# Kernel tuning notes

Hardware: AMD Instinct MI355X
Metric: run time of the kernel (lower is better)

## Reference

```python
import jax, jax.numpy as jnp
import numpy as np

EMB_DIM = 128
HEAD_SIZE = 16  # embDim // numHea = 128 // 8


def setup_inputs() -> dict:
    key = jax.random.key(0)
    k1, k2, k3, k4 = jax.random.split(key, 4)
    B, T = 8, 2048
    inpEmb = jax.random.normal(k1, (B, T, EMB_DIM), dtype=jnp.float32)
    # nn.Linear(embDim, heaSiz, bias=False) weights, stored transposed so y = x @ W
    Wq = jax.random.normal(k2, (EMB_DIM, HEAD_SIZE), dtype=jnp.float32) / np.sqrt(EMB_DIM)
    Wk = jax.random.normal(k3, (EMB_DIM, HEAD_SIZE), dtype=jnp.float32) / np.sqrt(EMB_DIM)
    Wv = jax.random.normal(k4, (EMB_DIM, HEAD_SIZE), dtype=jnp.float32) / np.sqrt(EMB_DIM)
    return {"inpEmb": inpEmb, "Wq": Wq, "Wk": Wk, "Wv": Wv}


def reference(inpEmb, Wq, Wk, Wv):
    # q,k,v: [B, T, H]
    q = inpEmb @ Wq
    k = inpEmb @ Wk
    v = inpEmb @ Wv
    scale = HEAD_SIZE ** -0.5
    # scores: [B, T, T]
    scores = jnp.einsum('bqh,bkh->bqk', q, k) * scale
    T = inpEmb.shape[1]
    causal = jnp.tril(jnp.ones((T, T), dtype=bool))
    scores = jnp.where(causal, scores, -jnp.inf)
    weights = jax.nn.softmax(scores, axis=-1)
    # dropout treated as identity (eval mode) for deterministic reference
    return jnp.einsum('bqk,bkh->bqh', weights, v)
```

## Files before the change

### kernel.cpp

```cpp
#include <hip/hip_runtime.h>
#include <hip/hip_bf16.h>

#define T_SEQ 2048
#define EMB   128
#define H     16
#define BATCH 8
#define BQ    64

typedef short short8_t __attribute__((ext_vector_type(8)));
typedef float f32x4    __attribute__((ext_vector_type(4)));

__device__ __forceinline__ unsigned short f2bf(float f) {
    __hip_bfloat16 h = __float2bfloat16(f);
    return *reinterpret_cast<unsigned short*>(&h);
}

__global__ __launch_bounds__(256) void qkv_kernel(
    const float* __restrict__ x,
    const float* __restrict__ Wq,
    const float* __restrict__ Wk,
    const float* __restrict__ Wv,
    unsigned short* __restrict__ Qbf,
    unsigned short* __restrict__ Kbf,
    unsigned short* __restrict__ Vt)
{
    __shared__ float Wt[3][16][132];

    const int tid = threadIdx.x;
    const int r0  = blockIdx.x * 32;

#pragma unroll
    for (int p = 0; p < 6; ++p) {
        const int idx4 = tid + p * 256;
        const int flat = idx4 * 4;
        const int mm   = flat >> 11;
        const int rem  = flat & 2047;
        const int d    = rem >> 4;
        const int c0   = rem & 15;
        const float* Wm = (mm == 0) ? Wq : (mm == 1) ? Wk : Wv;
        float4 w = *reinterpret_cast<const float4*>(Wm + rem);
        Wt[mm][c0    ][d] = w.x;
        Wt[mm][c0 + 1][d] = w.y;
        Wt[mm][c0 + 2][d] = w.z;
        Wt[mm][c0 + 3][d] = w.w;
    }
    __syncthreads();

    const int col  = tid & 15;
    const int rg   = tid >> 4;
    const int rowA = r0 + 2 * rg;
    const int rowB = rowA + 1;
    const float* xA = x + (size_t)rowA * EMB;
    const float* xB = x + (size_t)rowB * EMB;

    float qa0 = 0.f, ka0 = 0.f, va0 = 0.f;
    float qa1 = 0.f, ka1 = 0.f, va1 = 0.f;
#pragma unroll
    for (int d0 = 0; d0 < 128; d0 += 4) {
        float4 a  = *reinterpret_cast<const float4*>(xA + d0);
        float4 bb = *reinterpret_cast<const float4*>(xB + d0);
        float4 wq = *reinterpret_cast<const float4*>(&Wt[0][col][d0]);
        float4 wk = *reinterpret_cast<const float4*>(&Wt[1][col][d0]);
        float4 wv = *reinterpret_cast<const float4*>(&Wt[2][col][d0]);
        qa0 += a.x*wq.x + a.y*wq.y + a.z*wq.z + a.w*wq.w;
        ka0 += a.x*wk.x + a.y*wk.y + a.z*wk.z + a.w*wk.w;
        va0 += a.x*wv.x + a.y*wv.y + a.z*wv.z + a.w*wv.w;
        qa1 += bb.x*wq.x + bb.y*wq.y + bb.z*wq.z + bb.w*wq.w;
        ka1 += bb.x*wk.x + bb.y*wk.y + bb.z*wk.z + bb.w*wk.w;
        va1 += bb.x*wv.x + bb.y*wv.y + bb.z*wv.z + bb.w*wv.w;
    }
    const int bA = rowA >> 11, iA = rowA & 2047;
    const int bB = rowB >> 11, iB = rowB & 2047;
    Qbf[(size_t)rowA * H + col] = f2bf(qa0 * 0.25f);
    Kbf[(size_t)rowA * H + col] = f2bf(ka0);
    Vt[((size_t)bA * H + col) * T_SEQ + iA] = f2bf(va0);
    Qbf[(size_t)rowB * H + col] = f2bf(qa1 * 0.25f);
    Kbf[(size_t)rowB * H + col] = f2bf(ka1);
    Vt[((size_t)bB * H + col) * T_SEQ + iB] = f2bf(va1);
}

__global__ __launch_bounds__(256) void attn_phase1(
    const unsigned short* __restrict__ Qbf,
    const unsigned short* __restrict__ Kbf,
    const unsigned short* __restrict__ Vt,
    float* __restrict__ P2, int cs, int maxp)
{
    __shared__ unsigned int Pbuf[4][32][17];

    const int qt   = blockIdx.x;
    const int cch  = blockIdx.y;
    const int b    = blockIdx.z;
    const int i0   = qt * BQ;
    const int kbeg = cch << cs;
    if (kbeg >= i0 + BQ) return;

    const int tid  = threadIdx.x;
    const int w    = tid >> 6;
    const int lane = tid & 63;
    const int q    = lane >> 4;
    const int n    = lane & 15;
    const int irow = i0 + w * 16 + n;
    const int kend = min(kbeg + (1 << cs), i0 + w * 16 + 16);
    const int ntiles = (kend - kbeg + 63) >> 6;

    const unsigned short* Qp = Qbf + (size_t)b * T_SEQ * H;
    const unsigned short* Kp = Kbf + (size_t)b * T_SEQ * H;
    const unsigned short* Vp = Vt  + (size_t)b * H * T_SEQ;

    short8_t qf = {0,0,0,0,0,0,0,0};
    if (q < 2)
        qf = *reinterpret_cast<const short8_t*>(Qp + (size_t)irow * H + q * 8);

    f32x4 acc = {0.f, 0.f, 0.f, 0.f};
    float m = -1e30f, l = 0.f;

    for (int kt = 0; kt < ntiles; ++kt) {
        const int j0 = kbeg + kt * 64;

        f32x4 S[4];
#pragma unroll
        for (int s = 0; s < 4; ++s) {
            short8_t kf = {0,0,0,0,0,0,0,0};
            if (q < 2)
                kf = *reinterpret_cast<const short8_t*>(
                        Kp + (size_t)(j0 + s * 16 + n) * H + q * 8);
            f32x4 z = {0.f, 0.f, 0.f, 0.f};
            S[s] = __builtin_amdgcn_mfma_f32_16x16x32_bf16(kf, qf, z, 0, 0, 0);
        }

        float tm = -1e30f;
#pragma unroll
        for (int s = 0; s < 4; ++s) {
            const int kb = j0 + s * 16 + q * 4;
#pragma unroll
            for (int r = 0; r < 4; ++r) {
                float v = (kb + r <= irow) ? S[s][r] : -1e30f;
                S[s][r] = v;
                tm = fmaxf(tm, v);
            }
        }
        tm = fmaxf(tm, __shfl_xor(tm, 16));
        tm = fmaxf(tm, __shfl_xor(tm, 32));
        const float mn    = fmaxf(m, tm);
        const float alpha = __expf(m - mn);
        m = mn;

        float ps = 0.f;
#pragma unroll
        for (int s = 0; s < 4; ++s) {
            float e0 = __expf(S[s][0] - mn);
            float e1 = __expf(S[s][1] - mn);
            float e2 = __expf(S[s][2] - mn);
            float e3 = __expf(S[s][3] - mn);
            ps += (e0 + e1) + (e2 + e3);
            unsigned int b0 = __builtin_bit_cast(unsigned int, e0);
            unsigned int b1 = __builtin_bit_cast(unsigned int, e1);
            unsigned int b2 = __builtin_bit_cast(unsigned int, e2);
            unsigned int b3 = __builtin_bit_cast(unsigned int, e3);
            Pbuf[w][s * 8 + q * 2 + 0][n] = (b1 & 0xffff0000u) | (b0 >> 16);
            Pbuf[w][s * 8 + q * 2 + 1][n] = (b3 & 0xffff0000u) | (b2 >> 16);
        }
        ps += __shfl_xor(ps, 16);
        ps += __shfl_xor(ps, 32);
        l = l * alpha + ps;
        acc[0] *= alpha; acc[1] *= alpha; acc[2] *= alpha; acc[3] *= alpha;

#pragma unroll
        for (int h = 0; h < 2; ++h) {
            short8_t vf = *reinterpret_cast<const short8_t*>(
                    Vp + (size_t)n * T_SEQ + (j0 + h * 32 + q * 8));
            union { unsigned int u[4]; short8_t v; } pu;
            pu.u[0] = Pbuf[w][h * 16 + q * 4 + 0][n];
            pu.u[1] = Pbuf[w][h * 16 + q * 4 + 1][n];
            pu.u[2] = Pbuf[w][h * 16 + q * 4 + 2][n];
            pu.u[3] = Pbuf[w][h * 16 + q * 4 + 3][n];
            acc = __builtin_amdgcn_mfma_f32_16x16x32_bf16(vf, pu.v, acc, 0, 0, 0);
        }
    }

    float* pp = P2 + ((size_t)(b * T_SEQ + irow) * maxp + cch) * 18;
    float2 r01; r01.x = acc[0]; r01.y = acc[1];
    float2 r23; r23.x = acc[2]; r23.y = acc[3];
    *reinterpret_cast<float2*>(pp + q * 4)     = r01;
    *reinterpret_cast<float2*>(pp + q * 4 + 2) = r23;
    if (q == 0) { pp[16] = m; pp[17] = l; }
}

__global__ __launch_bounds__(256) void attn_phase2(
    const float* __restrict__ P2, float* __restrict__ out, int cs, int maxp)
{
    const int gid = blockIdx.x * 256 + threadIdx.x;
    const int row = gid >> 4;
    const int d   = gid & 15;
    const int ib  = row & (T_SEQ - 1);
    const int nc  = (ib >> cs) + 1;
    const float* base = P2 + (size_t)row * maxp * 18;

    float M = -1e30f;
    for (int p = 0; p < nc; ++p) M = fmaxf(M, base[p * 18 + 16]);
    float L = 0.f, o = 0.f;
    for (int p = 0; p < nc; ++p) {
        const float wgt = __expf(base[p * 18 + 16] - M);
        L += wgt * base[p * 18 + 17];
        o += wgt * base[p * 18 + d];
    }
    out[gid] = o / L;
}

extern "C" void kernel_launch(void* const* d_in, const int* in_sizes, int n_in,
                              void* d_out, int out_size, void* d_ws, size_t ws_size,
                              hipStream_t stream)
{
    const float* x  = (const float*)d_in[0];
    const float* Wq = (const float*)d_in[1];
    const float* Wk = (const float*)d_in[2];
    const float* Wv = (const float*)d_in[3];
    float* out = (float*)d_out;

    const size_t NE = (size_t)BATCH * T_SEQ * H;
    unsigned short* Qbf = (unsigned short*)d_ws;
    unsigned short* Kbf = Qbf + NE;
    unsigned short* Vt  = Kbf + NE;
    float* P2 = (float*)(Vt + NE);

    const size_t need8 = 3 * NE * 2 + (size_t)BATCH * T_SEQ * 8 * 18 * 4;
    int cs, maxp;
    if (ws_size >= need8) { cs = 8; maxp = 8; }
    else                  { cs = 9; maxp = 4; }

    qkv_kernel<<<BATCH * T_SEQ / 32, 256, 0, stream>>>(x, Wq, Wk, Wv, Qbf, Kbf, Vt);
    attn_phase1<<<dim3(T_SEQ / BQ, maxp, BATCH), 256, 0, stream>>>(
        Qbf, Kbf, Vt, P2, cs, maxp);
    attn_phase2<<<(int)(NE / 256), 256, 0, stream>>>(P2, out, cs, maxp);
}
```

Baseline: 90.29 us.

## Use MFMA for QKV projection, exp2 softmax, skip masking on full tiles

The QKV projection moves from scalar FP32 dot products to bf16 MFMA, with weights stored as bf16 in shared memory and 64 rows per block. The Q scale now folds in log2(e), so the softmax uses the hardware exp2 instead of expf. Causal masking is skipped for tiles that lie entirely below the diagonal, and V loads are hoisted ahead of the softmax so their latency overlaps it. Casting x and W to bf16 lowers projection precision.

```diff
diff --git a/kernel.cpp b/kernel.cpp
--- a/kernel.cpp
+++ b/kernel.cpp
@@ -6,6 +6,9 @@
 #define H     16
 #define BATCH 8
 #define BQ    64
+#define QSCALE 0.360673760222241f
+
+#define EXP2F(x) __builtin_amdgcn_exp2f(x)
 
 typedef short short8_t __attribute__((ext_vector_type(8)));
 typedef float f32x4    __attribute__((ext_vector_type(4)));
@@ -24,11 +27,9 @@
     unsigned short* __restrict__ Kbf,
     unsigned short* __restrict__ Vt)
 {
-    __shared__ float Wt[3][16][132];
+    __shared__ unsigned short Wt[3][16][136];
 
     const int tid = threadIdx.x;
-    const int r0  = blockIdx.x * 32;
-
 #pragma unroll
     for (int p = 0; p < 6; ++p) {
         const int idx4 = tid + p * 256;
@@ -39,44 +40,49 @@
         const int c0   = rem & 15;
         const float* Wm = (mm == 0) ? Wq : (mm == 1) ? Wk : Wv;
         float4 w = *reinterpret_cast<const float4*>(Wm + rem);
-        Wt[mm][c0    ][d] = w.x;
-        Wt[mm][c0 + 1][d] = w.y;
-        Wt[mm][c0 + 2][d] = w.z;
-        Wt[mm][c0 + 3][d] = w.w;
+        Wt[mm][c0    ][d] = f2bf(w.x);
+        Wt[mm][c0 + 1][d] = f2bf(w.y);
+        Wt[mm][c0 + 2][d] = f2bf(w.z);
+        Wt[mm][c0 + 3][d] = f2bf(w.w);
     }
     __syncthreads();
 
-    const int col  = tid & 15;
-    const int rg   = tid >> 4;
-    const int rowA = r0 + 2 * rg;
-    const int rowB = rowA + 1;
-    const float* xA = x + (size_t)rowA * EMB;
-    const float* xB = x + (size_t)rowB * EMB;
-
-    float qa0 = 0.f, ka0 = 0.f, va0 = 0.f;
-    float qa1 = 0.f, ka1 = 0.f, va1 = 0.f;
-#pragma unroll
-    for (int d0 = 0; d0 < 128; d0 += 4) {
-        float4 a  = *reinterpret_cast<const float4*>(xA + d0);
-        float4 bb = *reinterpret_cast<const float4*>(xB + d0);
-        float4 wq = *reinterpret_cast<const float4*>(&Wt[0][col][d0]);
-        float4 wk = *reinterpret_cast<const float4*>(&Wt[1][col][d0]);
-        float4 wv = *reinterpret_cast<const float4*>(&Wt[2][col][d0]);
-        qa0 += a.x*wq.x + a.y*wq.y + a.z*wq.z + a.w*wq.w;
-        ka0 += a.x*wk.x + a.y*wk.y + a.z*wk.z + a.w*wk.w;
-        va0 += a.x*wv.x + a.y*wv.y + a.z*wv.z + a.w*wv.w;
-        qa1 += bb.x*wq.x + bb.y*wq.y + bb.z*wq.z + bb.w*wq.w;
-        ka1 += bb.x*wk.x + bb.y*wk.y + bb.z*wk.z + bb.w*wk.w;
-        va1 += bb.x*wv.x + bb.y*wv.y + bb.z*wv.z + bb.w*wv.w;
-    }
-    const int bA = rowA >> 11, iA = rowA & 2047;
-    const int bB = rowB >> 11, iB = rowB & 2047;
-    Qbf[(size_t)rowA * H + col] = f2bf(qa0 * 0.25f);
-    Kbf[(size_t)rowA * H + col] = f2bf(ka0);
-    Vt[((size_t)bA * H + col) * T_SEQ + iA] = f2bf(va0);
-    Qbf[(size_t)rowB * H + col] = f2bf(qa1 * 0.25f);
-    Kbf[(size_t)rowB * H + col] = f2bf(ka1);
-    Vt[((size_t)bB * H + col) * T_SEQ + iB] = f2bf(va1);
+    const int w4   = tid >> 6;
+    const int lane = tid & 63;
+    const int q    = lane >> 4;
+    const int n    = lane & 15;
+    const int row0 = blockIdx.x * 64 + w4 * 16;
+    const float* xr = x + (size_t)(row0 + n) * EMB;
+
+    f32x4 aq = {0,0,0,0}, ak = {0,0,0,0}, av = {0,0,0,0};
+#pragma unroll
+    for (int t = 0; t < 4; ++t) {
+        const int k0 = t * 32 + q * 8;
+        float4 xa = *reinterpret_cast<const float4*>(xr + k0);
+        float4 xb = *reinterpret_cast<const float4*>(xr + k0 + 4);
+        union { unsigned short s[8]; short8_t v; } xf;
+        xf.s[0]=f2bf(xa.x); xf.s[1]=f2bf(xa.y); xf.s[2]=f2bf(xa.z); xf.s[3]=f2bf(xa.w);
+        xf.s[4]=f2bf(xb.x); xf.s[5]=f2bf(xb.y); xf.s[6]=f2bf(xb.z); xf.s[7]=f2bf(xb.w);
+        short8_t wqf = *reinterpret_cast<const short8_t*>(&Wt[0][n][k0]);
+        short8_t wkf = *reinterpret_cast<const short8_t*>(&Wt[1][n][k0]);
+        short8_t wvf = *reinterpret_cast<const short8_t*>(&Wt[2][n][k0]);
+        aq = __builtin_amdgcn_mfma_f32_16x16x32_bf16(xf.v, wqf, aq, 0, 0, 0);
+        ak = __builtin_amdgcn_mfma_f32_16x16x32_bf16(xf.v, wkf, ak, 0, 0, 0);
+        av = __builtin_amdgcn_mfma_f32_16x16x32_bf16(xf.v, wvf, av, 0, 0, 0);
+    }
+
+    const int grow = row0 + q * 4;
+    const int b    = grow >> 11;
+    const int ib0  = grow & 2047;
+#pragma unroll
+    for (int r = 0; r < 4; ++r) {
+        Qbf[(size_t)(grow + r) * H + n] = f2bf(aq[r] * QSCALE);
+        Kbf[(size_t)(grow + r) * H + n] = f2bf(ak[r]);
+    }
+    union { unsigned short s[4]; unsigned long long u; } vp;
+    vp.s[0]=f2bf(av[0]); vp.s[1]=f2bf(av[1]); vp.s[2]=f2bf(av[2]); vp.s[3]=f2bf(av[3]);
+    *reinterpret_cast<unsigned long long*>(
+        Vt + ((size_t)b * H + n) * T_SEQ + ib0) = vp.u;
 }
 
 __global__ __launch_bounds__(256) void attn_phase1(
@@ -99,8 +105,9 @@
     const int lane = tid & 63;
     const int q    = lane >> 4;
     const int n    = lane & 15;
-    const int irow = i0 + w * 16 + n;
-    const int kend = min(kbeg + (1 << cs), i0 + w * 16 + 16);
+    const int wrow0 = i0 + w * 16;
+    const int irow  = wrow0 + n;
+    const int kend  = min(kbeg + (1 << cs), wrow0 + 16);
     const int ntiles = (kend - kbeg + 63) >> 6;
 
     const unsigned short* Qp = Qbf + (size_t)b * T_SEQ * H;
@@ -128,30 +135,43 @@
             S[s] = __builtin_amdgcn_mfma_f32_16x16x32_bf16(kf, qf, z, 0, 0, 0);
         }
 
+        short8_t vf0 = *reinterpret_cast<const short8_t*>(
+                Vp + (size_t)n * T_SEQ + (j0 + q * 8));
+        short8_t vf1 = *reinterpret_cast<const short8_t*>(
+                Vp + (size_t)n * T_SEQ + (j0 + 32 + q * 8));
+
         float tm = -1e30f;
-#pragma unroll
-        for (int s = 0; s < 4; ++s) {
-            const int kb = j0 + s * 16 + q * 4;
-#pragma unroll
-            for (int r = 0; r < 4; ++r) {
-                float v = (kb + r <= irow) ? S[s][r] : -1e30f;
-                S[s][r] = v;
-                tm = fmaxf(tm, v);
+        if (j0 + 63 > wrow0) {
+#pragma unroll
+            for (int s = 0; s < 4; ++s) {
+                const int kb = j0 + s * 16 + q * 4;
+#pragma unroll
+                for (int r = 0; r < 4; ++r) {
+                    float v = (kb + r <= irow) ? S[s][r] : -1e30f;
+                    S[s][r] = v;
+                    tm = fmaxf(tm, v);
+                }
+            }
+        } else {
+#pragma unroll
+            for (int s = 0; s < 4; ++s) {
+                tm = fmaxf(tm, fmaxf(fmaxf(S[s][0], S[s][1]),
+                                     fmaxf(S[s][2], S[s][3])));
             }
         }
         tm = fmaxf(tm, __shfl_xor(tm, 16));
         tm = fmaxf(tm, __shfl_xor(tm, 32));
         const float mn    = fmaxf(m, tm);
-        const float alpha = __expf(m - mn);
+        const float alpha = EXP2F(m - mn);
         m = mn;
 
         float ps = 0.f;
 #pragma unroll
         for (int s = 0; s < 4; ++s) {
-            float e0 = __expf(S[s][0] - mn);
-            float e1 = __expf(S[s][1] - mn);
-            float e2 = __expf(S[s][2] - mn);
-            float e3 = __expf(S[s][3] - mn);
+            float e0 = EXP2F(S[s][0] - mn);
+            float e1 = EXP2F(S[s][1] - mn);
+            float e2 = EXP2F(S[s][2] - mn);
+            float e3 = EXP2F(S[s][3] - mn);
             ps += (e0 + e1) + (e2 + e3);
             unsigned int b0 = __builtin_bit_cast(unsigned int, e0);
             unsigned int b1 = __builtin_bit_cast(unsigned int, e1);
@@ -165,16 +185,18 @@
         l = l * alpha + ps;
         acc[0] *= alpha; acc[1] *= alpha; acc[2] *= alpha; acc[3] *= alpha;
 
-#pragma unroll
-        for (int h = 0; h < 2; ++h) {
-            short8_t vf = *reinterpret_cast<const short8_t*>(
-                    Vp + (size_t)n * T_SEQ + (j0 + h * 32 + q * 8));
+        {
             union { unsigned int u[4]; short8_t v; } pu;
-            pu.u[0] = Pbuf[w][h * 16 + q * 4 + 0][n];
-            pu.u[1] = Pbuf[w][h * 16 + q * 4 + 1][n];
-            pu.u[2] = Pbuf[w][h * 16 + q * 4 + 2][n];
-            pu.u[3] = Pbuf[w][h * 16 + q * 4 + 3][n];
-            acc = __builtin_amdgcn_mfma_f32_16x16x32_bf16(vf, pu.v, acc, 0, 0, 0);
+            pu.u[0] = Pbuf[w][q * 4 + 0][n];
+            pu.u[1] = Pbuf[w][q * 4 + 1][n];
+            pu.u[2] = Pbuf[w][q * 4 + 2][n];
+            pu.u[3] = Pbuf[w][q * 4 + 3][n];
+            acc = __builtin_amdgcn_mfma_f32_16x16x32_bf16(vf0, pu.v, acc, 0, 0, 0);
+            pu.u[0] = Pbuf[w][16 + q * 4 + 0][n];
+            pu.u[1] = Pbuf[w][16 + q * 4 + 1][n];
+            pu.u[2] = Pbuf[w][16 + q * 4 + 2][n];
+            pu.u[3] = Pbuf[w][16 + q * 4 + 3][n];
+            acc = __builtin_amdgcn_mfma_f32_16x16x32_bf16(vf1, pu.v, acc, 0, 0, 0);
         }
     }
 
@@ -200,7 +222,7 @@
     for (int p = 0; p < nc; ++p) M = fmaxf(M, base[p * 18 + 16]);
     float L = 0.f, o = 0.f;
     for (int p = 0; p < nc; ++p) {
-        const float wgt = __expf(base[p * 18 + 16] - M);
+        const float wgt = EXP2F(base[p * 18 + 16] - M);
         L += wgt * base[p * 18 + 17];
         o += wgt * base[p * 18 + d];
     }
@@ -228,7 +250,7 @@
     if (ws_size >= need8) { cs = 8; maxp = 8; }
     else                  { cs = 9; maxp = 4; }
 
-    qkv_kernel<<<BATCH * T_SEQ / 32, 256, 0, stream>>>(x, Wq, Wk, Wv, Qbf, Kbf, Vt);
+    qkv_kernel<<<BATCH * T_SEQ / 64, 256, 0, stream>>>(x, Wq, Wk, Wv, Qbf, Kbf, Vt);
     attn_phase1<<<dim3(T_SEQ / BQ, maxp, BATCH), 256, 0, stream>>>(
         Qbf, Kbf, Vt, P2, cs, maxp);
     attn_phase2<<<(int)(NE / 256), 256, 0, stream>>>(P2, out, cs, maxp);
```

Measured after the change: 89.79 us. No clear change (-0.6%).
